# Optimization experiments

Measured on AMD Instinct MI355X. Metric: run time of the kernel, lower is better.

## Reference

```python
import jax, jax.numpy as jnp
import numpy as np

DIM, INNER, NH = 256, 64, 8
HD = INNER // NH  # 8
B, H, W = 2, 48, 48
EPS = 1e-6


def _ln2d(x, w, b):
    # channel-first LayerNorm over dim=1, biased variance (matches LayerNorm2d)
    u = x.mean(axis=1, keepdims=True)
    s = ((x - u) ** 2).mean(axis=1, keepdims=True)
    xn = (x - u) / jnp.sqrt(s + EPS)
    return w[None, :, None, None] * xn + b[None, :, None, None]


def _conv1x1(x, w, b):
    return jnp.einsum('oc,bchw->bohw', w, x) + b[None, :, None, None]


def _attn(q, k, v):
    # q,k,v: [B, INNER, H, W] -> global attention over HW tokens per head
    Bq, C, Hh, Ww = q.shape
    split = lambda t: t.reshape(Bq, NH, HD, Hh * Ww)
    q, k, v = split(q), split(k), split(v)
    scale = HD ** -0.5
    attn = jnp.einsum('bhdn,bhdm->bhnm', q, k) * scale  # [B,nh,HW,HW]
    attn = jax.nn.softmax(attn, axis=-1)
    out = jnp.einsum('bhnm,bhdm->bhdn', attn, v)
    return out.reshape(Bq, C, Hh, Ww)


def setup_inputs() -> dict:
    key = jax.random.key(0)
    ks = jax.random.split(key, 12)
    w = lambda k, o, i: jax.random.normal(k, (o, i), dtype=jnp.float32) * 0.02
    d = {
        'f_rgb': jax.random.normal(ks[0], (B, DIM, H, W), dtype=jnp.float32),
        'f_ir': jax.random.normal(ks[1], (B, DIM, H, W), dtype=jnp.float32),
        'nr_w': jnp.ones(DIM), 'nr_b': jnp.zeros(DIM),
        'ni_w': jnp.ones(DIM), 'ni_b': jnp.zeros(DIM),
        'qr_w': w(ks[2], INNER, DIM), 'qr_b': jnp.zeros(INNER),
        'kvi_w': w(ks[3], 2 * INNER, DIM), 'kvi_b': jnp.zeros(2 * INNER),
        'qi_w': w(ks[4], INNER, DIM), 'qi_b': jnp.zeros(INNER),
        'kvr_w': w(ks[5], 2 * INNER, DIM), 'kvr_b': jnp.zeros(2 * INNER),
        'pr_w': w(ks[6], DIM, INNER), 'pr_b': jnp.zeros(DIM),
        'pr_lnw': jnp.ones(DIM), 'pr_lnb': jnp.zeros(DIM),
        'pi_w': w(ks[7], DIM, INNER), 'pi_b': jnp.zeros(DIM),
        'pi_lnw': jnp.ones(DIM), 'pi_lnb': jnp.zeros(DIM),
        'gr_w': w(ks[8], DIM, 2 * DIM), 'gr_b': jnp.zeros(DIM),
        'gi_w': w(ks[9], DIM, 2 * DIM), 'gi_b': jnp.zeros(DIM),
    }
    return d


def reference(f_rgb, f_ir, nr_w, nr_b, ni_w, ni_b, qr_w, qr_b, kvi_w, kvi_b,
              qi_w, qi_b, kvr_w, kvr_b, pr_w, pr_b, pr_lnw, pr_lnb,
              pi_w, pi_b, pi_lnw, pi_lnb, gr_w, gr_b, gi_w, gi_b):
    n_rgb = _ln2d(f_rgb, nr_w, nr_b)
    n_ir = _ln2d(f_ir, ni_w, ni_b)

    # RGB queries attend to IR keys/values
    q_r = _conv1x1(n_rgb, qr_w, qr_b)
    kv_i = _conv1x1(n_ir, kvi_w, kvi_b)
    k_i, v_i = kv_i[:, :INNER], kv_i[:, INNER:]
    rgb_cross = _attn(q_r, k_i, v_i)
    rgb_cross = _ln2d(_conv1x1(rgb_cross, pr_w, pr_b), pr_lnw, pr_lnb)
    gate_r = jax.nn.sigmoid(_conv1x1(jnp.concatenate([f_rgb, rgb_cross], axis=1), gr_w, gr_b))
    f_rgb_out = f_rgb + gate_r * rgb_cross

    # IR queries attend to RGB keys/values
    q_i = _conv1x1(n_ir, qi_w, qi_b)
    kv_r = _conv1x1(n_rgb, kvr_w, kvr_b)
    k_r, v_r = kv_r[:, :INNER], kv_r[:, INNER:]
    ir_cross = _attn(q_i, k_r, v_r)
    ir_cross = _ln2d(_conv1x1(ir_cross, pi_w, pi_b), pi_lnw, pi_lnb)
    gate_i = jax.nn.sigmoid(_conv1x1(jnp.concatenate([f_ir, ir_cross], axis=1), gi_w, gi_b))
    f_ir_out = f_ir + gate_i * ir_cross

    return (f_rgb_out, f_ir_out)
```

## Files before the change

kernel.cpp:

```cpp
#include <hip/hip_runtime.h>

static constexpr int kDim   = 256;
static constexpr int kInner = 64;
static constexpr int kNH    = 8;
static constexpr int kB     = 2;
static constexpr int kP     = 2304;
static constexpr float kScale = 0.35355339059327373f;
static constexpr float kEps   = 1e-6f;

typedef __fp16   fp16x2 __attribute__((ext_vector_type(2)));
typedef _Float16 half4f __attribute__((ext_vector_type(4)));
typedef _Float16 half8  __attribute__((ext_vector_type(8)));
typedef float    f32x4  __attribute__((ext_vector_type(4)));

static constexpr size_t oXq  = 0;
static constexpr size_t oQ16 = 2359296;
static constexpr size_t oK16 = 2949120;
static constexpr size_t oV16 = 3538944;
static constexpr size_t oA16 = 4128768;
static constexpr size_t oW16 = 7077888;
static constexpr size_t kInpStride = 294912;

__global__ __launch_bounds__(256) void prep(
    const float* __restrict__ x0, const float* __restrict__ w0,
    const float* __restrict__ b0, const float* __restrict__ x1,
    const float* __restrict__ w1, const float* __restrict__ b1,
    _Float16* __restrict__ Xq,
    const float* __restrict__ qr_w, const float* __restrict__ kvr_w,
    const float* __restrict__ qi_w, const float* __restrict__ kvi_w,
    const float* __restrict__ pr_w, const float* __restrict__ pi_w,
    const float* __restrict__ gr_w, const float* __restrict__ gi_w,
    _Float16* __restrict__ w16)
{
    if (blockIdx.x >= 576) {
        const int flat = blockIdx.x - 576;
        const int y = flat >> 6, x = flat & 63;
        const float* src; _Float16* dst; int n;
        _Float16* Aq = w16;
        _Float16* Ap = w16 + 98304;
        _Float16* Ag = w16 + 131072;
        switch (y) {
            case 0: src = qr_w;  dst = Aq;          n = 16384;  break;
            case 1: src = kvr_w; dst = Aq + 16384;  n = 32768;  break;
            case 2: src = qi_w;  dst = Aq + 49152;  n = 16384;  break;
            case 3: src = kvi_w; dst = Aq + 65536;  n = 32768;  break;
            case 4: src = pr_w;  dst = Ap;          n = 16384;  break;
            case 5: src = pi_w;  dst = Ap + 16384;  n = 16384;  break;
            case 6: src = gr_w;  dst = Ag;          n = 131072; break;
            default:src = gi_w;  dst = Ag + 131072; n = 131072; break;
        }
        for (int i = x * 256 + threadIdx.x; i < n; i += 64 * 256)
            dst[i] = (_Float16)src[i];
        return;
    }
    __shared__ float sb[16][16];
    __shared__ float ssb[16][16];
    const int fid = blockIdx.x;
    const int xcd = fid & 7, q = fid >> 3;
    const int inp = (xcd >> 2) & 1, bb = (xcd >> 1) & 1, half = xcd & 1;
    const float* x = inp ? x1 : x0;
    const float* w = inp ? w1 : w0;
    const float* b = inp ? b1 : b0;
    const int pos = threadIdx.x & 15;
    const int grp = threadIdx.x >> 4;
    const int p   = half * 1152 + q * 16 + pos;
    const size_t base = (size_t)bb * kDim * kP + p;
    const int c0 = grp * 16;

    float v[16];
    float s = 0.f, ss = 0.f;
    #pragma unroll
    for (int j = 0; j < 16; ++j) {
        v[j] = x[base + (size_t)(c0 + j) * kP];
        s += v[j]; ss += v[j] * v[j];
    }
    sb[grp][pos] = s; ssb[grp][pos] = ss;
    __syncthreads();
    float st = 0.f, sst = 0.f;
    #pragma unroll
    for (int g = 0; g < 16; ++g) { st += sb[g][pos]; sst += ssb[g][pos]; }
    const float mean = st * (1.f / kDim);
    const float rstd = rsqrtf(sst * (1.f / kDim) - mean * mean + kEps);
    half8 h0, h1;
    #pragma unroll
    for (int j = 0; j < 8; ++j) {
        h0[j] = (_Float16)((v[j]     - mean) * rstd * w[c0 + j]     + b[c0 + j]);
        h1[j] = (_Float16)((v[j + 8] - mean) * rstd * w[c0 + j + 8] + b[c0 + j + 8]);
    }
    _Float16* dst = Xq + ((size_t)(inp * 2 + bb) * kP + p) * 256 + c0;
    *(half8*)dst       = h0;
    *(half8*)(dst + 8) = h1;
}

template <int M, int K, int EPI>
__global__ __launch_bounds__(256) void gemm_f16(
    const _Float16* __restrict__ A,
    const _Float16* __restrict__ B,
    const float* __restrict__ b0, const float* __restrict__ b1,
    const float* __restrict__ b2, const float* __restrict__ b3,
    _Float16* __restrict__ o16a, _Float16* __restrict__ o16b, _Float16* __restrict__ o16c,
    const float* __restrict__ f0, const float* __restrict__ f1,
    float* __restrict__ outp)
{
    constexpr int MT64 = M / 64;
    const int fid = blockIdx.x;
    const int xcd = fid & 7, q = fid >> 3;
    const int s = (xcd >> 2) & 1, bb = (xcd >> 1) & 1, half = xcd & 1;
    const int ot64 = (q % MT64) * 64;
    const int pt   = q / MT64;
    const int wv = threadIdx.x >> 6, lane = threadIdx.x & 63;
    const int r16 = lane & 15, g = lane >> 4;
    const int ot = ot64 + wv * 16;
    const int p0 = half * 1152 + pt * 64;
    const int combo = s * 2 + bb;

    const _Float16* Ar = A + ((size_t)s * M + ot + r16) * K + 8 * g;
    const _Float16* Br = B + ((size_t)combo * kP + p0 + r16) * K + 8 * g;
    f32x4 acc0[4], acc1[4];
    #pragma unroll
    for (int ps = 0; ps < 4; ++ps) {
        acc0[ps] = (f32x4){0.f, 0.f, 0.f, 0.f};
        acc1[ps] = (f32x4){0.f, 0.f, 0.f, 0.f};
    }
    #pragma unroll 4
    for (int c0 = 0; c0 < K; c0 += 32) {
        const half8 a8 = *(const half8*)(Ar + c0);
        half8 b8[4];
        #pragma unroll
        for (int ps = 0; ps < 4; ++ps)
            b8[ps] = *(const half8*)(Br + (size_t)(16 * ps) * K + c0);
        const half4f al = {a8[0], a8[1], a8[2], a8[3]};
        const half4f ah = {a8[4], a8[5], a8[6], a8[7]};
        #pragma unroll
        for (int ps = 0; ps < 4; ++ps) {
            const half4f bl = {b8[ps][0], b8[ps][1], b8[ps][2], b8[ps][3]};
            const half4f bh = {b8[ps][4], b8[ps][5], b8[ps][6], b8[ps][7]};
            acc0[ps] = __builtin_amdgcn_mfma_f32_16x16x16f16(al, bl, acc0[ps], 0, 0, 0);
            acc1[ps] = __builtin_amdgcn_mfma_f32_16x16x16f16(ah, bh, acc1[ps], 0, 0, 0);
        }
    }
    const int obase = ot + 4 * g;

    #pragma unroll
    for (int ps = 0; ps < 4; ++ps) {
        float acc[4];
        #pragma unroll
        for (int i = 0; i < 4; ++i) acc[i] = acc0[ps][i] + acc1[ps][i];
        const int p = p0 + 16 * ps + r16;

        if constexpr (EPI == 0) {
            const int dlo = 4 * (g & 1);
            if (ot < 64) {
                const float* qb = s ? b1 : b0;
                const float4 bv = *(const float4*)(qb + obase);
                const int h = (ot >> 3) + (g >> 1);
                half4f o = { (_Float16)((acc[0] + bv.x) * kScale), (_Float16)((acc[1] + bv.y) * kScale),
                             (_Float16)((acc[2] + bv.z) * kScale), (_Float16)((acc[3] + bv.w) * kScale) };
                *(half4f*)(o16a + (((size_t)combo * 8 + h) * kP + p) * 8 + dlo) = o;
            } else if (ot < 128) {
                const float* kb = s ? b3 : b2;
                const float4 bv = *(const float4*)(kb + obase - 64);
                const int h = ((ot - 64) >> 3) + (g >> 1);
                half4f o = { (_Float16)(acc[0] + bv.x), (_Float16)(acc[1] + bv.y),
                             (_Float16)(acc[2] + bv.z), (_Float16)(acc[3] + bv.w) };
                *(half4f*)(o16b + (((size_t)combo * 8 + h) * kP + p) * 8 + dlo) = o;
            } else {
                const float* kb = s ? b3 : b2;
                const float4 bv = *(const float4*)(kb + obase - 64);
                const int h = ((ot - 128) >> 3) + (g >> 1);
                const float* bvp = (const float*)&bv;
                #pragma unroll
                for (int i = 0; i < 4; ++i)
                    o16c[(((size_t)combo * 8 + h) * 8 + dlo + i) * kP + p] = (_Float16)(acc[i] + bvp[i]);
            }
        } else {
            const float* gb = s ? b1 : b0;
            const float4 bv = *(const float4*)(gb + obase);
            const float* bvp = (const float*)&bv;
            const half4f cx = *(const half4f*)(B + ((size_t)combo * kP + p) * 512 + 256 + obase);
            const float* F = s ? f1 : f0;
            #pragma unroll
            for (int i = 0; i < 4; ++i) {
                const int o = obase + i;
                const float gt = 1.f / (1.f + __expf(-(acc[i] + bvp[i])));
                const float fb = F[((size_t)bb * kDim + o) * kP + p];
                outp[((size_t)combo * kDim + o) * kP + p] = fb + gt * (float)cx[i];
            }
        }
    }
}

__global__ __launch_bounds__(256) void proj_ln(
    const _Float16* __restrict__ a16, const _Float16* __restrict__ Ap,
    const float* __restrict__ pb0, const float* __restrict__ pb1,
    const float* __restrict__ w0, const float* __restrict__ b0,
    const float* __restrict__ w1, const float* __restrict__ b1,
    const float* __restrict__ f0, const float* __restrict__ f1,
    _Float16* __restrict__ Xg)
{
    __shared__ float sb[4][4][16];
    __shared__ float ssb[4][4][16];
    const int fid = blockIdx.x;
    const int xcd = fid & 7, q = fid >> 3;
    const int s = (xcd >> 2) & 1, bb = (xcd >> 1) & 1, half = xcd & 1;
    const int wv = threadIdx.x >> 6, lane = threadIdx.x & 63;
    const int r16 = lane & 15, g = lane >> 4;
    const int p = half * 1152 + q * 16 + r16;
    const int combo = s * 2 + bb;
    const float* pb = s ? pb1 : pb0;
    const float* w  = s ? w1 : w0;
    const float* b  = s ? b1 : b0;
    const float* F  = s ? f1 : f0;

    const _Float16* Br = a16 + ((size_t)combo * kP + p) * 64 + 8 * g;
    const half8 bA = *(const half8*)Br;
    const half8 bB = *(const half8*)(Br + 32);
    const half4f bl0 = {bA[0], bA[1], bA[2], bA[3]};
    const half4f bh0 = {bA[4], bA[5], bA[6], bA[7]};
    const half4f bl1 = {bB[0], bB[1], bB[2], bB[3]};
    const half4f bh1 = {bB[4], bB[5], bB[6], bB[7]};

    float cval[4][4];
    float psum = 0.f, psq = 0.f;
    #pragma unroll
    for (int t = 0; t < 4; ++t) {
        const int ot = wv * 64 + t * 16;
        const _Float16* Ar = Ap + ((size_t)s * 256 + ot + r16) * 64 + 8 * g;
        const half8 aA = *(const half8*)Ar;
        const half8 aB = *(const half8*)(Ar + 32);
        const half4f al0 = {aA[0], aA[1], aA[2], aA[3]};
        const half4f ah0 = {aA[4], aA[5], aA[6], aA[7]};
        const half4f al1 = {aB[0], aB[1], aB[2], aB[3]};
        const half4f ah1 = {aB[4], aB[5], aB[6], aB[7]};
        f32x4 acc0 = __builtin_amdgcn_mfma_f32_16x16x16f16(al0, bl0, (f32x4){0.f,0.f,0.f,0.f}, 0, 0, 0);
        acc0 = __builtin_amdgcn_mfma_f32_16x16x16f16(al1, bl1, acc0, 0, 0, 0);
        f32x4 acc1 = __builtin_amdgcn_mfma_f32_16x16x16f16(ah0, bh0, (f32x4){0.f,0.f,0.f,0.f}, 0, 0, 0);
        acc1 = __builtin_amdgcn_mfma_f32_16x16x16f16(ah1, bh1, acc1, 0, 0, 0);
        const float4 bv = *(const float4*)(pb + ot + 4 * g);
        const float* bvp = (const float*)&bv;
        #pragma unroll
        for (int i = 0; i < 4; ++i) {
            const float v = acc0[i] + acc1[i] + bvp[i];
            cval[t][i] = v;
            psum += v; psq += v * v;
        }
    }
    sb[wv][g][r16] = psum; ssb[wv][g][r16] = psq;
    __syncthreads();
    float st = 0.f, sst = 0.f;
    #pragma unroll
    for (int w2 = 0; w2 < 4; ++w2)
        #pragma unroll
        for (int g2 = 0; g2 < 4; ++g2) { st += sb[w2][g2][r16]; sst += ssb[w2][g2][r16]; }
    const float mean = st * (1.f / kDim);
    const float rstd = rsqrtf(sst * (1.f / kDim) - mean * mean + kEps);

    _Float16* xrow = Xg + ((size_t)combo * kP + p) * 512;
    #pragma unroll
    for (int t = 0; t < 4; ++t) {
        const int o4 = wv * 64 + t * 16 + 4 * g;
        const float4 lw = *(const float4*)(w + o4);
        const float4 lb = *(const float4*)(b + o4);
        const float* lwp = (const float*)&lw;
        const float* lbp = (const float*)&lb;
        half4f o;
        #pragma unroll
        for (int i = 0; i < 4; ++i)
            o[i] = (_Float16)((cval[t][i] - mean) * rstd * lwp[i] + lbp[i]);
        *(half4f*)(xrow + 256 + o4) = o;
        half4f r;
        #pragma unroll
        for (int i = 0; i < 4; ++i)
            r[i] = (_Float16)F[((size_t)bb * kDim + o4 + i) * kP + p];
        *(half4f*)(xrow + o4) = r;
    }
}

__global__ __launch_bounds__(256) void attn_mfma(
    const _Float16* __restrict__ q16, const _Float16* __restrict__ k16,
    const _Float16* __restrict__ vt16, _Float16* __restrict__ a16)
{
    __shared__ _Float16 Ksm[16 * 64 * 4];
    __shared__ _Float16 Vsm[16 * 66 * 4];
    const int st = blockIdx.z;
    const _Float16* Qg = q16  + (size_t)st * kInpStride;
    const _Float16* Kg = k16  + (size_t)(1 - st) * kInpStride;
    const _Float16* Vg = vt16 + (size_t)(1 - st) * kInpStride;
    const int bh = blockIdx.y;
    const int bb = bh >> 3, h = bh & 7;
    const int tid  = threadIdx.x;
    const int wv   = tid >> 6;
    const int lane = tid & 63;
    const int r16  = lane & 15;
    const int g    = lane >> 4;

    #pragma unroll
    for (int j = 0; j < 2; ++j) {
        const int s = tid + 256 * j;
        const int kt = s >> 5, m = s & 31;
        *(half4f*)(Ksm + (kt * 64 + 32 + m) * 4) = (half4f){0, 0, 0, 0};
        const int rv = 8 + (m & 7), gv = m >> 3;
        const half4f vv = (rv == 8)
            ? (half4f){(_Float16)1.f, (_Float16)1.f, (_Float16)1.f, (_Float16)1.f}
            : (half4f){0, 0, 0, 0};
        *(half4f*)(Vsm + (kt * 66 + gv * 16 + rv) * 4) = vv;
    }

    const int qg = blockIdx.x * 64 + wv * 16 + r16;
    half4f qf = (half4f){0, 0, 0, 0};
    if (g < 2) qf = *(const half4f*)(Qg + ((size_t)bh * kP + qg) * 8 + g * 4);

    const int vd = tid >> 5, vc8 = (tid & 31) * 8;
    const int vkt = vc8 >> 4, vgv = (vc8 & 15) >> 2;
    _Float16* kdst = Ksm + ((tid >> 4) * 64 + (tid & 15)) * 4;
    _Float16* vdst = Vsm + (vkt * 66 + vgv * 16 + vd) * 4;
    const _Float16* ksrc = Kg + ((size_t)bh * kP + tid) * 8;
    const _Float16* vsrc = Vg + (size_t)(bh * 8 + vd) * kP + vc8;

    half8 kreg = *(const half8*)ksrc;
    half8 vreg = *(const half8*)vsrc;

    f32x4 of0 = (f32x4){0.f, 0.f, 0.f, 0.f};
    f32x4 of1 = (f32x4){0.f, 0.f, 0.f, 0.f};

    for (int ch = 0; ch < 9; ++ch) {
        if (ch) __syncthreads();
        *(half4f*)kdst        = (half4f){kreg[0], kreg[1], kreg[2], kreg[3]};
        *(half4f*)(kdst + 64) = (half4f){kreg[4], kreg[5], kreg[6], kreg[7]};
        *(half4f*)vdst        = (half4f){vreg[0], vreg[1], vreg[2], vreg[3]};
        *(half4f*)(vdst + 64) = (half4f){vreg[4], vreg[5], vreg[6], vreg[7]};
        __syncthreads();
        if (ch < 8) {
            kreg = *(const half8*)(ksrc + (size_t)(ch + 1) * 2048);
            vreg = *(const half8*)(vsrc + (size_t)(ch + 1) * 256);
        }
        #pragma unroll
        for (int kt = 0; kt < 16; ++kt) {
            const half4f kf = *(const half4f*)(Ksm + (kt * 64 + lane) * 4);
            f32x4 sv = __builtin_amdgcn_mfma_f32_16x16x16f16(kf, qf, (f32x4){0.f,0.f,0.f,0.f}, 0, 0, 0);
            const float e0 = __expf(sv[0]), e1 = __expf(sv[1]);
            const float e2 = __expf(sv[2]), e3 = __expf(sv[3]);
            const fp16x2 lo = __builtin_amdgcn_cvt_pkrtz(e0, e1);
            const fp16x2 hi = __builtin_amdgcn_cvt_pkrtz(e2, e3);
            const half4f pf = { (_Float16)lo[0], (_Float16)lo[1],
                                (_Float16)hi[0], (_Float16)hi[1] };
            const half4f vf = *(const half4f*)(Vsm + (kt * 66 + lane) * 4);
            if (kt & 1) of1 = __builtin_amdgcn_mfma_f32_16x16x16f16(vf, pf, of1, 0, 0, 0);
            else        of0 = __builtin_amdgcn_mfma_f32_16x16x16f16(vf, pf, of0, 0, 0, 0);
        }
    }
    const f32x4 of = of0 + of1;
    const float rsv = __shfl(of[0], 32 + r16, 64);
    const float inv = 1.f / rsv;
    if (g < 2) {
        half4f o = { (_Float16)(of[0] * inv), (_Float16)(of[1] * inv),
                     (_Float16)(of[2] * inv), (_Float16)(of[3] * inv) };
        *(half4f*)(a16 + ((size_t)(st * 2 + bb) * kP + qg) * 64 + h * 8 + g * 4) = o;
    }
}

extern "C" void kernel_launch(void* const* d_in, const int* in_sizes, int n_in,
                              void* d_out, int out_size, void* d_ws, size_t ws_size,
                              hipStream_t stream)
{
    const float* f_rgb  = (const float*)d_in[0];
    const float* f_ir   = (const float*)d_in[1];
    const float* nr_w   = (const float*)d_in[2];
    const float* nr_b   = (const float*)d_in[3];
    const float* ni_w   = (const float*)d_in[4];
    const float* ni_b   = (const float*)d_in[5];
    const float* qr_w   = (const float*)d_in[6];
    const float* qr_b   = (const float*)d_in[7];
    const float* kvi_w  = (const float*)d_in[8];
    const float* kvi_b  = (const float*)d_in[9];
    const float* qi_w   = (const float*)d_in[10];
    const float* qi_b   = (const float*)d_in[11];
    const float* kvr_w  = (const float*)d_in[12];
    const float* kvr_b  = (const float*)d_in[13];
    const float* pr_w   = (const float*)d_in[14];
    const float* pr_b   = (const float*)d_in[15];
    const float* pr_lnw = (const float*)d_in[16];
    const float* pr_lnb = (const float*)d_in[17];
    const float* pi_w   = (const float*)d_in[18];
    const float* pi_b   = (const float*)d_in[19];
    const float* pi_lnw = (const float*)d_in[20];
    const float* pi_lnb = (const float*)d_in[21];
    const float* gr_w   = (const float*)d_in[22];
    const float* gr_b   = (const float*)d_in[23];
    const float* gi_w   = (const float*)d_in[24];
    const float* gi_b   = (const float*)d_in[25];

    _Float16* hb   = (_Float16*)d_ws;
    _Float16* Xq   = hb + oXq;
    _Float16* q16  = hb + oQ16;
    _Float16* k16  = hb + oK16;
    _Float16* vt16 = hb + oV16;
    _Float16* a16  = hb + oA16;
    _Float16* Xg   = hb;
    _Float16* W16  = hb + oW16;
    _Float16* Aq   = W16;
    _Float16* Ap   = W16 + 98304;
    _Float16* Ag   = W16 + 131072;

    float* outp = (float*)d_out;
    const dim3 blk(256);

    prep<<<dim3(1088), blk, 0, stream>>>(f_rgb, nr_w, nr_b, f_ir, ni_w, ni_b, Xq,
                                         qr_w, kvr_w, qi_w, kvi_w, pr_w, pi_w, gr_w, gi_w, W16);
    gemm_f16<192, 256, 0><<<dim3(432), blk, 0, stream>>>(
        Aq, Xq, qr_b, qi_b, kvr_b, kvi_b, q16, k16, vt16, nullptr, nullptr, nullptr);
    attn_mfma<<<dim3(36, 16, 2), blk, 0, stream>>>(q16, k16, vt16, a16);
    proj_ln<<<dim3(576), blk, 0, stream>>>(a16, Ap, pr_b, pi_b,
                                           pr_lnw, pr_lnb, pi_lnw, pi_lnb,
                                           f_rgb, f_ir, Xg);
    gemm_f16<256, 512, 2><<<dim3(576), blk, 0, stream>>>(
        Ag, Xg, gr_b, gi_b, nullptr, nullptr, nullptr, nullptr, nullptr, f_rgb, f_ir, outp);
}
```

Baseline: 101.8 us.

## Double-buffer attention K/V tiles and vectorize LayerNorm prep with wider blocks

The attention kernel now keeps two shared-memory K/V buffers, so the next chunk is written to the other buffer after compute and one barrier per chunk is dropped. The prep LayerNorm switches to float4 loads covering 32 positions per block, with a two-stage reduction through shared memory. Block counts for both the normalization and the weight-cast blocks are reduced. Shared memory use in attention doubles, which may lower occupancy, and prep now has fewer, larger blocks.

After: 105.9 us. 4.0% more time.

```diff
diff --git a/kernel.cpp b/kernel.cpp
--- a/kernel.cpp
+++ b/kernel.cpp
@@ -32,9 +32,9 @@
     const float* __restrict__ gr_w, const float* __restrict__ gi_w,
     _Float16* __restrict__ w16)
 {
-    if (blockIdx.x >= 576) {
-        const int flat = blockIdx.x - 576;
-        const int y = flat >> 6, x = flat & 63;
+    if (blockIdx.x >= 288) {
+        const int flat = blockIdx.x - 288;
+        const int y = flat >> 4, x = flat & 15;
         const float* src; _Float16* dst; int n;
         _Float16* Aq = w16;
         _Float16* Ap = w16 + 98304;
@@ -49,47 +49,68 @@
             case 6: src = gr_w;  dst = Ag;          n = 131072; break;
             default:src = gi_w;  dst = Ag + 131072; n = 131072; break;
         }
-        for (int i = x * 256 + threadIdx.x; i < n; i += 64 * 256)
+        for (int i = x * 256 + threadIdx.x; i < n; i += 16 * 256)
             dst[i] = (_Float16)src[i];
         return;
     }
-    __shared__ float sb[16][16];
-    __shared__ float ssb[16][16];
+    __shared__ float sb[32][33];
+    __shared__ float ssb[32][33];
+    __shared__ float mrs[2][32];
     const int fid = blockIdx.x;
     const int xcd = fid & 7, q = fid >> 3;
     const int inp = (xcd >> 2) & 1, bb = (xcd >> 1) & 1, half = xcd & 1;
     const float* x = inp ? x1 : x0;
     const float* w = inp ? w1 : w0;
     const float* b = inp ? b1 : b0;
-    const int pos = threadIdx.x & 15;
-    const int grp = threadIdx.x >> 4;
-    const int p   = half * 1152 + q * 16 + pos;
-    const size_t base = (size_t)bb * kDim * kP + p;
-    const int c0 = grp * 16;
-
-    float v[16];
-    float s = 0.f, ss = 0.f;
-    #pragma unroll
-    for (int j = 0; j < 16; ++j) {
-        v[j] = x[base + (size_t)(c0 + j) * kP];
-        s += v[j]; ss += v[j] * v[j];
-    }
-    sb[grp][pos] = s; ssb[grp][pos] = ss;
+    const int px = threadIdx.x & 7;
+    const int cg = threadIdx.x >> 3;
+    const int p0 = half * 1152 + q * 32;
+    const int pbase = p0 + px * 4;
+    const size_t base = (size_t)bb * kDim * kP;
+    const int c0 = cg * 8;
+
+    float4 v4[8];
+    float ps0 = 0.f, ps1 = 0.f, ps2 = 0.f, ps3 = 0.f;
+    float pq0 = 0.f, pq1 = 0.f, pq2 = 0.f, pq3 = 0.f;
+    #pragma unroll
+    for (int j = 0; j < 8; ++j) {
+        v4[j] = *(const float4*)(x + base + (size_t)(c0 + j) * kP + pbase);
+        ps0 += v4[j].x; pq0 += v4[j].x * v4[j].x;
+        ps1 += v4[j].y; pq1 += v4[j].y * v4[j].y;
+        ps2 += v4[j].z; pq2 += v4[j].z * v4[j].z;
+        ps3 += v4[j].w; pq3 += v4[j].w * v4[j].w;
+    }
+    *(float4*)&sb[cg][px * 4]  = make_float4(ps0, ps1, ps2, ps3);
+    *(float4*)&ssb[cg][px * 4] = make_float4(pq0, pq1, pq2, pq3);
     __syncthreads();
-    float st = 0.f, sst = 0.f;
-    #pragma unroll
-    for (int g = 0; g < 16; ++g) { st += sb[g][pos]; sst += ssb[g][pos]; }
-    const float mean = st * (1.f / kDim);
-    const float rstd = rsqrtf(sst * (1.f / kDim) - mean * mean + kEps);
-    half8 h0, h1;
-    #pragma unroll
-    for (int j = 0; j < 8; ++j) {
-        h0[j] = (_Float16)((v[j]     - mean) * rstd * w[c0 + j]     + b[c0 + j]);
-        h1[j] = (_Float16)((v[j + 8] - mean) * rstd * w[c0 + j + 8] + b[c0 + j + 8]);
-    }
-    _Float16* dst = Xq + ((size_t)(inp * 2 + bb) * kP + p) * 256 + c0;
-    *(half8*)dst       = h0;
-    *(half8*)(dst + 8) = h1;
+    if (threadIdx.x < 32) {
+        const int p = threadIdx.x;
+        float s = 0.f, ss = 0.f;
+        #pragma unroll 8
+        for (int g2 = 0; g2 < 32; ++g2) { s += sb[g2][p]; ss += ssb[g2][p]; }
+        const float mean = s * (1.f / kDim);
+        mrs[0][p] = mean;
+        mrs[1][p] = rsqrtf(ss * (1.f / kDim) - mean * mean + kEps);
+    }
+    __syncthreads();
+    const float4 w4a = *(const float4*)(w + c0);
+    const float4 w4b = *(const float4*)(w + c0 + 4);
+    const float4 b4a = *(const float4*)(b + c0);
+    const float4 b4b = *(const float4*)(b + c0 + 4);
+    const float wv[8] = {w4a.x, w4a.y, w4a.z, w4a.w, w4b.x, w4b.y, w4b.z, w4b.w};
+    const float bv[8] = {b4a.x, b4a.y, b4a.z, b4a.w, b4b.x, b4b.y, b4b.z, b4b.w};
+    #pragma unroll
+    for (int i = 0; i < 4; ++i) {
+        const float mean = mrs[0][px * 4 + i];
+        const float rstd = mrs[1][px * 4 + i];
+        half8 h;
+        #pragma unroll
+        for (int j = 0; j < 8; ++j) {
+            const float vj = ((const float*)&v4[j])[i];
+            h[j] = (_Float16)((vj - mean) * rstd * wv[j] + bv[j]);
+        }
+        *(half8*)(Xq + ((size_t)(inp * 2 + bb) * kP + pbase + i) * 256 + c0) = h;
+    }
 }
 
 template <int M, int K, int EPI>
@@ -280,8 +301,8 @@
     const _Float16* __restrict__ q16, const _Float16* __restrict__ k16,
     const _Float16* __restrict__ vt16, _Float16* __restrict__ a16)
 {
-    __shared__ _Float16 Ksm[16 * 64 * 4];
-    __shared__ _Float16 Vsm[16 * 66 * 4];
+    __shared__ _Float16 Ksm[2][16 * 64 * 4];
+    __shared__ _Float16 Vsm[2][16 * 66 * 4];
     const int st = blockIdx.z;
     const _Float16* Qg = q16  + (size_t)st * kInpStride;
     const _Float16* Kg = k16  + (size_t)(1 - st) * kInpStride;
@@ -295,15 +316,16 @@
     const int g    = lane >> 4;
 
     #pragma unroll
-    for (int j = 0; j < 2; ++j) {
+    for (int j = 0; j < 4; ++j) {
         const int s = tid + 256 * j;
-        const int kt = s >> 5, m = s & 31;
-        *(half4f*)(Ksm + (kt * 64 + 32 + m) * 4) = (half4f){0, 0, 0, 0};
+        const int buf = s >> 9, s2 = s & 511;
+        const int kt = s2 >> 5, m = s2 & 31;
+        *(half4f*)(Ksm[buf] + (kt * 64 + 32 + m) * 4) = (half4f){0, 0, 0, 0};
         const int rv = 8 + (m & 7), gv = m >> 3;
-        const half4f vv = (rv == 8)
+        const half4f vvp = (rv == 8)
             ? (half4f){(_Float16)1.f, (_Float16)1.f, (_Float16)1.f, (_Float16)1.f}
             : (half4f){0, 0, 0, 0};
-        *(half4f*)(Vsm + (kt * 66 + gv * 16 + rv) * 4) = vv;
+        *(half4f*)(Vsm[buf] + (kt * 66 + gv * 16 + rv) * 4) = vvp;
     }
 
     const int qg = blockIdx.x * 64 + wv * 16 + r16;
@@ -312,31 +334,35 @@
 
     const int vd = tid >> 5, vc8 = (tid & 31) * 8;
     const int vkt = vc8 >> 4, vgv = (vc8 & 15) >> 2;
-    _Float16* kdst = Ksm + ((tid >> 4) * 64 + (tid & 15)) * 4;
-    _Float16* vdst = Vsm + (vkt * 66 + vgv * 16 + vd) * 4;
+    const int koff = ((tid >> 4) * 64 + (tid & 15)) * 4;
+    const int voff = (vkt * 66 + vgv * 16 + vd) * 4;
     const _Float16* ksrc = Kg + ((size_t)bh * kP + tid) * 8;
     const _Float16* vsrc = Vg + (size_t)(bh * 8 + vd) * kP + vc8;
 
-    half8 kreg = *(const half8*)ksrc;
-    half8 vreg = *(const half8*)vsrc;
+    {
+        const half8 k8 = *(const half8*)ksrc;
+        const half8 v8 = *(const half8*)vsrc;
+        *(half4f*)(Ksm[0] + koff)      = (half4f){k8[0], k8[1], k8[2], k8[3]};
+        *(half4f*)(Ksm[0] + koff + 64) = (half4f){k8[4], k8[5], k8[6], k8[7]};
+        *(half4f*)(Vsm[0] + voff)      = (half4f){v8[0], v8[1], v8[2], v8[3]};
+        *(half4f*)(Vsm[0] + voff + 64) = (half4f){v8[4], v8[5], v8[6], v8[7]};
+    }
 
     f32x4 of0 = (f32x4){0.f, 0.f, 0.f, 0.f};
     f32x4 of1 = (f32x4){0.f, 0.f, 0.f, 0.f};
 
     for (int ch = 0; ch < 9; ++ch) {
-        if (ch) __syncthreads();
-        *(half4f*)kdst        = (half4f){kreg[0], kreg[1], kreg[2], kreg[3]};
-        *(half4f*)(kdst + 64) = (half4f){kreg[4], kreg[5], kreg[6], kreg[7]};
-        *(half4f*)vdst        = (half4f){vreg[0], vreg[1], vreg[2], vreg[3]};
-        *(half4f*)(vdst + 64) = (half4f){vreg[4], vreg[5], vreg[6], vreg[7]};
         __syncthreads();
+        half8 kreg, vreg;
         if (ch < 8) {
             kreg = *(const half8*)(ksrc + (size_t)(ch + 1) * 2048);
             vreg = *(const half8*)(vsrc + (size_t)(ch + 1) * 256);
         }
+        const _Float16* Kb = Ksm[ch & 1];
+        const _Float16* Vb = Vsm[ch & 1];
         #pragma unroll
         for (int kt = 0; kt < 16; ++kt) {
-            const half4f kf = *(const half4f*)(Ksm + (kt * 64 + lane) * 4);
+            const half4f kf = *(const half4f*)(Kb + (kt * 64 + lane) * 4);
             f32x4 sv = __builtin_amdgcn_mfma_f32_16x16x16f16(kf, qf, (f32x4){0.f,0.f,0.f,0.f}, 0, 0, 0);
             const float e0 = __expf(sv[0]), e1 = __expf(sv[1]);
             const float e2 = __expf(sv[2]), e3 = __expf(sv[3]);
@@ -344,9 +370,17 @@
             const fp16x2 hi = __builtin_amdgcn_cvt_pkrtz(e2, e3);
             const half4f pf = { (_Float16)lo[0], (_Float16)lo[1],
                                 (_Float16)hi[0], (_Float16)hi[1] };
-            const half4f vf = *(const half4f*)(Vsm + (kt * 66 + lane) * 4);
+            const half4f vf = *(const half4f*)(Vb + (kt * 66 + lane) * 4);
             if (kt & 1) of1 = __builtin_amdgcn_mfma_f32_16x16x16f16(vf, pf, of1, 0, 0, 0);
             else        of0 = __builtin_amdgcn_mfma_f32_16x16x16f16(vf, pf, of0, 0, 0, 0);
+        }
+        if (ch < 8) {
+            _Float16* Kn = Ksm[(ch + 1) & 1];
+            _Float16* Vn = Vsm[(ch + 1) & 1];
+            *(half4f*)(Kn + koff)      = (half4f){kreg[0], kreg[1], kreg[2], kreg[3]};
+            *(half4f*)(Kn + koff + 64) = (half4f){kreg[4], kreg[5], kreg[6], kreg[7]};
+            *(half4f*)(Vn + voff)      = (half4f){vreg[0], vreg[1], vreg[2], vreg[3]};
+            *(half4f*)(Vn + voff + 64) = (half4f){vreg[4], vreg[5], vreg[6], vreg[7]};
         }
     }
     const f32x4 of = of0 + of1;
@@ -405,8 +439,8 @@
     float* outp = (float*)d_out;
     const dim3 blk(256);
 
-    prep<<<dim3(1088), blk, 0, stream>>>(f_rgb, nr_w, nr_b, f_ir, ni_w, ni_b, Xq,
-                                         qr_w, kvr_w, qi_w, kvi_w, pr_w, pi_w, gr_w, gi_w, W16);
+    prep<<<dim3(416), blk, 0, stream>>>(f_rgb, nr_w, nr_b, f_ir, ni_w, ni_b, Xq,
+                                        qr_w, kvr_w, qi_w, kvi_w, pr_w, pi_w, gr_w, gi_w, W16);
     gemm_f16<192, 256, 0><<<dim3(432), blk, 0, stream>>>(
         Aq, Xq, qr_b, qi_b, kvr_b, kvi_b, q16, k16, vt16, nullptr, nullptr, nullptr);
     attn_mfma<<<dim3(36, 16, 2), blk, 0, stream>>>(q16, k16, vt16, a16);
```
